# Kernel tuning notes

Hardware: AMD Instinct MI355X
Metric: run time of the kernel (lower is better)

The kernel has to match this reference:

```python
import jax, jax.numpy as jnp
import numpy as np

B, N, C = 16, 1024, 256
NH, DH = 8, 32          # dense attention heads
NHD, P = 8, 4           # deformable heads / sampling points
Hs = Ws = 32            # value spatial grid (N == Hs*Ws)
HID = 1024              # mlp hidden = 4*C


def setup_inputs() -> dict:
    key = jax.random.key(0)
    ks = jax.random.split(key, 16)
    rn = lambda i, shape, s=1.0: jax.random.normal(ks[i], shape, jnp.float32) * s
    return {
        "x": rn(0, (B, N, C)),
        "ref": jax.random.uniform(ks[1], (B, N, 2), jnp.float32),
        "value": rn(2, (B, N, C)),
        "ln1_w": jnp.ones((C,), jnp.float32), "ln1_b": jnp.zeros((C,), jnp.float32),
        "ln2_w": jnp.ones((C,), jnp.float32), "ln2_b": jnp.zeros((C,), jnp.float32),
        "ln3_w": jnp.ones((C,), jnp.float32), "ln3_b": jnp.zeros((C,), jnp.float32),
        "qkv_w": rn(3, (3 * C, C), 0.05),
        "proj_w": rn(4, (C, C), 0.05), "proj_b": jnp.zeros((C,), jnp.float32),
        "off_w": rn(5, (NHD * P * 2, C), 0.01), "off_b": rn(6, (NHD * P * 2,), 0.5),
        "aw_w": rn(7, (NHD * P, C), 0.01), "aw_b": jnp.zeros((NHD * P,), jnp.float32),
        "vproj_w": rn(8, (C, C), 0.05), "vproj_b": jnp.zeros((C,), jnp.float32),
        "oproj_w": rn(9, (C, C), 0.05), "oproj_b": jnp.zeros((C,), jnp.float32),
        "fc1_w": rn(10, (HID, C), 0.05), "fc1_b": jnp.zeros((HID,), jnp.float32),
        "fc2_w": rn(11, (C, HID), 0.05), "fc2_b": jnp.zeros((C,), jnp.float32),
    }


def _ln(x, w, b):
    m = x.mean(-1, keepdims=True)
    v = ((x - m) ** 2).mean(-1, keepdims=True)
    return (x - m) * jax.lax.rsqrt(v + 1e-5) * w + b


def _attn(x, qkv_w, proj_w, proj_b):
    qkv = (x @ qkv_w.T).reshape(B, N, 3, NH, DH)
    q, k, v = qkv[:, :, 0], qkv[:, :, 1], qkv[:, :, 2]
    a = jnp.einsum('bqhd,bkhd->bhqk', q, k) * (DH ** -0.5)
    a = jax.nn.softmax(a, axis=-1)
    o = jnp.einsum('bhqk,bkhd->bqhd', a, v).reshape(B, N, C)
    return o @ proj_w.T + proj_b


def _deform(q, ref, value, off_w, off_b, aw_w, aw_b, vproj_w, vproj_b, oproj_w, oproj_b):
    # single-level MS deformable attention (Deformable-DETR style)
    v = (value @ vproj_w.T + vproj_b).reshape(B, Hs * Ws, NHD, DH)
    off = (q @ off_w.T + off_b).reshape(B, N, NHD, P, 2)
    aw = jax.nn.softmax((q @ aw_w.T + aw_b).reshape(B, N, NHD, P), axis=-1)
    norm = jnp.array([Ws, Hs], jnp.float32)
    loc = ref[:, :, None, None, :] + off / norm  # [B,N,NHD,P,2] normalized coords
    gx = loc[..., 0] * Ws - 0.5
    gy = loc[..., 1] * Hs - 0.5
    x0 = jnp.floor(gx); y0 = jnp.floor(gy)
    lx = gx - x0; ly = gy - y0
    x0i = x0.astype(jnp.int32); y0i = y0.astype(jnp.int32)
    b_idx = jnp.arange(B)[:, None, None, None]
    h_idx = jnp.arange(NHD)[None, None, :, None]

    def gather(xi, yi):
        valid = ((xi >= 0) & (xi < Ws) & (yi >= 0) & (yi < Hs)).astype(jnp.float32)
        idx = jnp.clip(yi, 0, Hs - 1) * Ws + jnp.clip(xi, 0, Ws - 1)
        return v[b_idx, idx, h_idx] * valid[..., None]  # [B,N,NHD,P,DH]

    s = (gather(x0i, y0i) * ((1 - lx) * (1 - ly))[..., None]
         + gather(x0i + 1, y0i) * (lx * (1 - ly))[..., None]
         + gather(x0i, y0i + 1) * ((1 - lx) * ly)[..., None]
         + gather(x0i + 1, y0i + 1) * (lx * ly)[..., None])
    out = (s * aw[..., None]).sum(axis=3).reshape(B, N, C)
    return out @ oproj_w.T + oproj_b


def reference(x, ref, value, ln1_w, ln1_b, ln2_w, ln2_b, ln3_w, ln3_b,
              qkv_w, proj_w, proj_b, off_w, off_b, aw_w, aw_b,
              vproj_w, vproj_b, oproj_w, oproj_b, fc1_w, fc1_b, fc2_w, fc2_b):
    x = x + _attn(_ln(x, ln1_w, ln1_b), qkv_w, proj_w, proj_b)
    x = x + _deform(_ln(x, ln2_w, ln2_b), ref, value,
                    off_w, off_b, aw_w, aw_b, vproj_w, vproj_b, oproj_w, oproj_b)
    h = jax.nn.gelu(_ln(x, ln3_w, ln3_b) @ fc1_w.T + fc1_b, approximate=False) @ fc2_w.T + fc2_b
    return x + h
```

## Files before the change

### kernel.cpp

```cpp
#include <hip/hip_runtime.h>
#include <hip/hip_bf16.h>

#define Bq   16
#define Nq   1024
#define Cq   256
#define NHq  8
#define DHq  32
#define HIDq 1024
#define BNq  (Bq * Nq)

typedef float f32x4 __attribute__((ext_vector_type(4)));
typedef short bf16x8 __attribute__((ext_vector_type(8)));
typedef unsigned short ushort_t;

__device__ __forceinline__ unsigned int f2bf(float f) {
    unsigned int u = __builtin_bit_cast(unsigned int, f);
    u = (u + 0x7fffu + ((u >> 16) & 1u)) >> 16;
    return u & 0xffffu;
}
__device__ __forceinline__ unsigned int packbf2(float a, float b) {
    unsigned int ua = __builtin_bit_cast(unsigned int, a) + 0x8000u;
    unsigned int ub = __builtin_bit_cast(unsigned int, b) + 0x8000u;
    return __builtin_amdgcn_perm(ub, ua, 0x07060302);
}
__device__ __forceinline__ float bflo(unsigned int u) { return __builtin_bit_cast(float, u << 16); }
__device__ __forceinline__ float bfhi(unsigned int u) { return __builtin_bit_cast(float, u & 0xffff0000u); }
__device__ __forceinline__ float gelu_t(float x) {
    float y = x * (0.7978845608028654f + 0.035677408136300125f * x * x);
    float e = __builtin_amdgcn_exp2f(y * 2.8853900817779268f);
    return x - x / (1.f + e);
}

typedef __attribute__((address_space(1))) const unsigned int* gas_u32;
typedef __attribute__((address_space(3))) unsigned int* las_u32;
__device__ __forceinline__ void gload16(const void* g, void* l) {
    __builtin_amdgcn_global_load_lds((gas_u32)g, (las_u32)l, 16, 0, 0);
}

struct CastSeg { const float* src; ushort_t* dst; int nblk; int n; };
struct CastArgs { CastSeg s[9]; };

__global__ __launch_bounds__(256) void castm(CastArgs a) {
    int bid = blockIdx.x;
    int seg = 0, acc = 0;
    for (seg = 0; seg < 9; seg++) {
        if (bid < acc + a.s[seg].nblk) break;
        acc += a.s[seg].nblk;
    }
    const CastSeg sg = a.s[seg];
    int i = (bid - acc) * 1024 + threadIdx.x * 4;
    if (i < sg.n) {
        float4 v = *(const float4*)(sg.src + i);
        uint2 u;
        u.x = packbf2(v.x, v.y);
        u.y = packbf2(v.z, v.w);
        *(uint2*)(sg.dst + i) = u;
    }
}

template <typename TI>
__global__ __launch_bounds__(256) void ln_kernel(const TI* __restrict__ X,
                                                 const float* __restrict__ w,
                                                 const float* __restrict__ b,
                                                 ushort_t* __restrict__ Y) {
    int wave = threadIdx.x >> 6, lane = threadIdx.x & 63;
    int t = blockIdx.x * 4 + wave;
    float4 v;
    if constexpr (sizeof(TI) == 4) {
        v = *(const float4*)((const float*)X + (size_t)t * Cq + lane * 4);
    } else {
        uint2 u = *(const uint2*)((const ushort_t*)X + (size_t)t * Cq + lane * 4);
        v = make_float4(bflo(u.x), bfhi(u.x), bflo(u.y), bfhi(u.y));
    }
    float s = v.x + v.y + v.z + v.w;
#pragma unroll
    for (int d = 1; d < 64; d <<= 1) s += __shfl_xor(s, d);
    float mean = s * (1.f / 256.f);
    float4 dv = {v.x - mean, v.y - mean, v.z - mean, v.w - mean};
    float q = dv.x * dv.x + dv.y * dv.y + dv.z * dv.z + dv.w * dv.w;
#pragma unroll
    for (int d = 1; d < 64; d <<= 1) q += __shfl_xor(q, d);
    float rs = rsqrtf(q * (1.f / 256.f) + 1e-5f);
    float4 wv = *(const float4*)(w + lane * 4);
    float4 bv = *(const float4*)(b + lane * 4);
    uint2 u;
    u.x = packbf2(dv.x * rs * wv.x + bv.x, dv.y * rs * wv.y + bv.y);
    u.y = packbf2(dv.z * rs * wv.z + bv.z, dv.w * rs * wv.w + bv.w);
    *(uint2*)(Y + (size_t)t * Cq + lane * 4) = u;
}

template <int OMODE, bool GELU_, bool RESID, int KT, int NT, typename RT>
__global__ __launch_bounds__(256) void mgemm(const ushort_t* __restrict__ A,
                                             const ushort_t* __restrict__ W,
                                             const float* __restrict__ bias,
                                             const void* __restrict__ R,
                                             void* __restrict__ OutP,
                                             int M, int Nn) {
    constexpr int NJ = NT / 32;
    __shared__ __align__(16) ushort_t Al[8192];
    __shared__ __align__(16) ushort_t Bl[NT * 64];
    int m0 = blockIdx.x * 128, n0 = blockIdx.y * NT;
    int tid = threadIdx.x;
    int w = tid >> 6, lane = tid & 63;
    int l15 = lane & 15, quad = lane >> 4;
    int wrow = w >> 1, wcol = w & 1;

    f32x4 acc[4][NJ];
#pragma unroll
    for (int i = 0; i < 4; i++)
#pragma unroll
        for (int j = 0; j < NJ; j++) acc[i][j] = (f32x4){0.f, 0.f, 0.f, 0.f};

    const ushort_t* gA0 = A + (size_t)(m0 + lane) * KT + w * 8;
    const ushort_t* gA1 = A + (size_t)(m0 + 64 + lane) * KT + w * 8;
    const ushort_t* gB0 = W + (size_t)(n0 + lane) * KT + w * 8;
    const ushort_t* gB1 = (NT == 128) ? W + (size_t)(n0 + 64 + lane) * KT + w * 8 : nullptr;
    ushort_t* lA0  = &Al[(w * 128) * 8];
    ushort_t* lA1  = &Al[(w * 128 + 64) * 8];
    ushort_t* lA0h = &Al[((w + 4) * 128) * 8];
    ushort_t* lA1h = &Al[((w + 4) * 128 + 64) * 8];
    ushort_t* lB0  = &Bl[(w * NT) * 8];
    ushort_t* lB0h = &Bl[((w + 4) * NT) * 8];
    ushort_t* lB1  = (NT == 128) ? &Bl[(w * NT + 64) * 8] : nullptr;
    ushort_t* lB1h = (NT == 128) ? &Bl[((w + 4) * NT + 64) * 8] : nullptr;

#pragma unroll
    for (int k0 = 0; k0 < KT; k0 += 64) {
        gload16(gA0 + k0, lA0);
        gload16(gA1 + k0, lA1);
        gload16(gA0 + k0 + 32, lA0h);
        gload16(gA1 + k0 + 32, lA1h);
        gload16(gB0 + k0, lB0);
        gload16(gB0 + k0 + 32, lB0h);
        if constexpr (NT == 128) {
            gload16(gB1 + k0, lB1);
            gload16(gB1 + k0 + 32, lB1h);
        }
        __syncthreads();

#pragma unroll
        for (int ks = 0; ks < 2; ks++) {
            bf16x8 aF[4], bF[NJ];
#pragma unroll
            for (int i = 0; i < 4; i++)
                aF[i] = *(const bf16x8*)&Al[((ks * 4 + quad) * 128 + wrow * 64 + i * 16 + l15) * 8];
#pragma unroll
            for (int j = 0; j < NJ; j++)
                bF[j] = *(const bf16x8*)&Bl[((ks * 4 + quad) * NT + wcol * (NT / 2) + j * 16 + l15) * 8];
#pragma unroll
            for (int i = 0; i < 4; i++)
#pragma unroll
                for (int j = 0; j < NJ; j++)
                    acc[i][j] = __builtin_amdgcn_mfma_f32_16x16x32_bf16(bF[j], aF[i], acc[i][j], 0, 0, 0);
        }
        __syncthreads();
    }

#pragma unroll
    for (int i = 0; i < 4; i++) {
        int mg = m0 + wrow * 64 + i * 16 + l15;
#pragma unroll
        for (int j = 0; j < NJ; j++) {
            int ng = n0 + wcol * (NT / 2) + j * 16 + quad * 4;
            f32x4 rv = acc[i][j];
            if constexpr (OMODE == 1) {
                int which = ng >> 8;
                int h = (ng >> 5) & 7;
                int d = ng & 31;
                int bb = mg >> 10, nn = mg & 1023;
                ushort_t* qb = (ushort_t*)OutP;
                if (which == 2) {
                    size_t dst = 2 * (size_t)BNq * Cq +
                                 ((size_t)(bb * 8 + h) * 32 + d) * 1024 + nn;
#pragma unroll
                    for (int r = 0; r < 4; r++)
                        qb[dst + (size_t)r * 1024] = (ushort_t)f2bf(rv[r]);
                } else {
                    if (which == 0) {
                        const float sc = 0.17677669529663687f * 1.4426950408889634f;
                        rv[0] *= sc; rv[1] *= sc; rv[2] *= sc; rv[3] *= sc;
                    }
                    size_t dst = (size_t)which * ((size_t)BNq * Cq) +
                                 ((size_t)(bb * 8 + h) * 1024 + nn) * 32 + d;
                    uint2 pk;
                    pk.x = packbf2(rv[0], rv[1]);
                    pk.y = packbf2(rv[2], rv[3]);
                    *(uint2*)(qb + dst) = pk;
                }
            } else if constexpr (OMODE == 3) {
                if (ng >= 96) continue;
                if (ng < 64) {
                    float4 bv = *(const float4*)(bias + ng);
                    rv[0] += bv.x; rv[1] += bv.y; rv[2] += bv.z; rv[3] += bv.w;
                    *(float4*)((float*)OutP + (size_t)mg * 64 + ng) =
                        make_float4(rv[0], rv[1], rv[2], rv[3]);
                } else {
                    float4 bv = *(const float4*)((const float*)R + (ng - 64));
                    rv[0] += bv.x; rv[1] += bv.y; rv[2] += bv.z; rv[3] += bv.w;
                    *(float4*)((float*)OutP + (size_t)BNq * 64 + (size_t)mg * 32 + (ng - 64)) =
                        make_float4(rv[0], rv[1], rv[2], rv[3]);
                }
            } else {
                if (bias) {
                    float4 bv = *(const float4*)(bias + ng);
                    rv[0] += bv.x; rv[1] += bv.y; rv[2] += bv.z; rv[3] += bv.w;
                }
                if (GELU_) {
#pragma unroll
                    for (int r = 0; r < 4; r++) rv[r] = gelu_t(rv[r]);
                }
                if (RESID) {
                    if constexpr (sizeof(RT) == 4) {
                        float4 rr = *(const float4*)((const float*)R + (size_t)mg * Nn + ng);
                        rv[0] += rr.x; rv[1] += rr.y; rv[2] += rr.z; rv[3] += rr.w;
                    } else {
                        uint2 ru = *(const uint2*)((const ushort_t*)R + (size_t)mg * Nn + ng);
                        rv[0] += bflo(ru.x); rv[1] += bfhi(ru.x);
                        rv[2] += bflo(ru.y); rv[3] += bfhi(ru.y);
                    }
                }
                if constexpr (OMODE == 2) {
                    uint2 pk;
                    pk.x = packbf2(rv[0], rv[1]);
                    pk.y = packbf2(rv[2], rv[3]);
                    *(uint2*)((ushort_t*)OutP + (size_t)mg * Nn + ng) = pk;
                } else {
                    *(float4*)((float*)OutP + (size_t)mg * Nn + ng) =
                        make_float4(rv[0], rv[1], rv[2], rv[3]);
                }
            }
        }
    }
}

__global__ __launch_bounds__(256) void attn_mfma(const ushort_t* __restrict__ Qb,
                                                 const ushort_t* __restrict__ Kb,
                                                 const ushort_t* __restrict__ Vtg,
                                                 ushort_t* __restrict__ o) {
    int bh = blockIdx.x;
    int b = bh >> 3, h = bh & 7;
    int q0 = blockIdx.y * 128;
    int tid = threadIdx.x;
    int wave = tid >> 6, lane = tid & 63;
    int l15 = lane & 15, quad = lane >> 4;

    __shared__ __align__(16) ushort_t Ks[64][40];
    __shared__ __align__(16) ushort_t Vs[32][88];
    __shared__ __align__(16) ushort_t Ps[4][32][72];

    const size_t hb = (size_t)bh * 32768;

    bf16x8 qfrag[2];
#pragma unroll
    for (int g = 0; g < 2; g++)
        qfrag[g] = *(const bf16x8*)(Qb + hb + (size_t)(q0 + wave * 32 + g * 16 + l15) * 32 + quad * 8);

    f32x4 oa[2][2];
#pragma unroll
    for (int g = 0; g < 2; g++)
#pragma unroll
        for (int t = 0; t < 2; t++) oa[g][t] = (f32x4){0.f, 0.f, 0.f, 0.f};
    float lsum[2] = {0.f, 0.f};

    int krow = tid >> 2, kch = tid & 3;
    int vrow = tid >> 3, vch = tid & 7;
    const ushort_t* kgp = Kb + hb + (size_t)krow * 32 + kch * 8;
    const ushort_t* vgp = Vtg + hb + (size_t)vrow * 1024 + vch * 8;

    for (int kt = 0; kt < 16; kt++) {
        __syncthreads();
        *(bf16x8*)&Ks[krow][kch * 8] = *(const bf16x8*)(kgp + kt * 64 * 32);
        *(bf16x8*)&Vs[vrow][vch * 8] = *(const bf16x8*)(vgp + kt * 64);
        __syncthreads();

        bf16x8 kf[4];
#pragma unroll
        for (int kg = 0; kg < 4; kg++)
            kf[kg] = *(const bf16x8*)&Ks[kg * 16 + l15][quad * 8];

        const f32x4 z = {0.f, 0.f, 0.f, 0.f};
#pragma unroll
        for (int g = 0; g < 2; g++) {
#pragma unroll
            for (int kg = 0; kg < 4; kg++) {
                f32x4 st = __builtin_amdgcn_mfma_f32_16x16x32_bf16(kf[kg], qfrag[g], z, 0, 0, 0);
                float e0 = __builtin_amdgcn_exp2f(st[0]);
                float e1 = __builtin_amdgcn_exp2f(st[1]);
                float e2 = __builtin_amdgcn_exp2f(st[2]);
                float e3 = __builtin_amdgcn_exp2f(st[3]);
                lsum[g] += (e0 + e1) + (e2 + e3);
                uint2 pk;
                pk.x = packbf2(e0, e1);
                pk.y = packbf2(e2, e3);
                *(uint2*)&Ps[wave][g * 16 + l15][kg * 16 + quad * 4] = pk;
            }
        }
#pragma unroll
        for (int c = 0; c < 2; c++) {
            bf16x8 vb0 = *(const bf16x8*)&Vs[l15][c * 32 + quad * 8];
            bf16x8 vb1 = *(const bf16x8*)&Vs[16 + l15][c * 32 + quad * 8];
#pragma unroll
            for (int g = 0; g < 2; g++) {
                bf16x8 pa = *(const bf16x8*)&Ps[wave][g * 16 + l15][c * 32 + quad * 8];
                oa[g][0] = __builtin_amdgcn_mfma_f32_16x16x32_bf16(pa, vb0, oa[g][0], 0, 0, 0);
                oa[g][1] = __builtin_amdgcn_mfma_f32_16x16x32_bf16(pa, vb1, oa[g][1], 0, 0, 0);
            }
        }
    }

#pragma unroll
    for (int g = 0; g < 2; g++) {
        float rs = lsum[g];
        rs += __shfl_xor(rs, 16);
        rs += __shfl_xor(rs, 32);
        lsum[g] = rs;
    }
#pragma unroll
    for (int g = 0; g < 2; g++) {
#pragma unroll
        for (int r = 0; r < 4; r++) {
            float inv = 1.f / __shfl(lsum[g], quad * 4 + r);
            int q = q0 + wave * 32 + g * 16 + quad * 4 + r;
            ushort_t* orow = o + ((size_t)(b * 1024 + q)) * 256 + h * 32;
            orow[l15] = (ushort_t)f2bf(oa[g][0][r] * inv);
            orow[l15 + 16] = (ushort_t)f2bf(oa[g][1][r] * inv);
        }
    }
}

__global__ __launch_bounds__(256) void deform_kernel(const float* __restrict__ ref,
                                                     const float* __restrict__ off,
                                                     const float* __restrict__ awl,
                                                     const ushort_t* __restrict__ v,
                                                     ushort_t* __restrict__ out) {
    int t = blockIdx.x;
    int b = t >> 10;
    int tid = threadIdx.x;
    int h = tid >> 5, d = tid & 31;

    float rx = ref[(size_t)t * 2 + 0];
    float ry = ref[(size_t)t * 2 + 1];
    const float* offr = off + (size_t)t * 64 + h * 8;
    const float* awr = awl + (size_t)t * 32 + h * 4;

    float L0 = awr[0], L1 = awr[1], L2 = awr[2], L3 = awr[3];
    float mm = fmaxf(fmaxf(L0, L1), fmaxf(L2, L3));
    float e0 = __expf(L0 - mm), e1 = __expf(L1 - mm), e2 = __expf(L2 - mm), e3 = __expf(L3 - mm);
    float inv = 1.f / (e0 + e1 + e2 + e3);
    float aw[4] = {e0 * inv, e1 * inv, e2 * inv, e3 * inv};

    const ushort_t* vb = v + (size_t)b * Nq * Cq + h * 32 + d;

    float s = 0.f;
#pragma unroll
    for (int p = 0; p < 4; p++) {
        float gx = rx * 32.f + offr[p * 2 + 0] - 0.5f;
        float gy = ry * 32.f + offr[p * 2 + 1] - 0.5f;
        float x0f = floorf(gx), y0f = floorf(gy);
        float lx = gx - x0f, ly = gy - y0f;
        int x0 = (int)x0f, y0 = (int)y0f;
        auto g = [&](int xi, int yi) -> float {
            if (xi < 0 || xi > 31 || yi < 0 || yi > 31) return 0.f;
            return bflo((unsigned int)vb[(size_t)(yi * 32 + xi) * Cq]);
        };
        float sp = g(x0, y0) * (1.f - lx) * (1.f - ly)
                 + g(x0 + 1, y0) * lx * (1.f - ly)
                 + g(x0, y0 + 1) * (1.f - lx) * ly
                 + g(x0 + 1, y0 + 1) * lx * ly;
        s += aw[p] * sp;
    }
    out[(size_t)t * Cq + h * 32 + d] = (ushort_t)f2bf(s);
}

extern "C" void kernel_launch(void* const* d_in, const int* in_sizes, int n_in,
                              void* d_out, int out_size, void* d_ws, size_t ws_size,
                              hipStream_t stream) {
    const size_t S = (size_t)BNq * Cq;
    float* ws = (float*)d_ws;
    ushort_t* Xbf = (ushort_t*)ws;
    ushort_t* Ybf = (ushort_t*)(ws + S / 2);
    ushort_t* Wbf = (ushort_t*)(ws + S);

    ushort_t* Wqkv   = Wbf;
    ushort_t* Wproj  = Wbf + 196608;
    ushort_t* Woff   = Wbf + 262144;
    ushort_t* Wvproj = Wbf + 286720;
    ushort_t* Woproj = Wbf + 352256;
    ushort_t* Wfc1   = Wbf + 417792;
    ushort_t* Wfc2   = Wbf + 679936;

    ushort_t* QKVbf = (ushort_t*)(ws + 2 * S);
    ushort_t* O1bf  = (ushort_t*)(ws + 2 * S + 3 * S / 2);
    ushort_t* Vbbf  = (ushort_t*)(ws + 2 * S);
    float* OffB = ws + 2 * S + S / 2;
    float* AwB  = OffB + (size_t)BNq * 64;
    ushort_t* Sbbf = (ushort_t*)(ws + 3 * S);
    ushort_t* Hbbf = (ushort_t*)(ws + 2 * S);
    ushort_t* Valbf = (ushort_t*)(ws + 9 * S / 2);

    auto fp = [&](int i) { return (const float*)d_in[i]; };
    const float* x_in = fp(0);

    CastArgs ca;
    ca.s[0] = {fp(9),  Wqkv,   192, 196608};
    ca.s[1] = {fp(10), Wproj,  64,  65536};
    ca.s[2] = {fp(12), Woff,   16,  16384};
    ca.s[3] = {fp(14), Wbf + 278528, 8, 8192};
    ca.s[4] = {fp(16), Wvproj, 64,  65536};
    ca.s[5] = {fp(18), Woproj, 64,  65536};
    ca.s[6] = {fp(20), Wfc1,   256, 262144};
    ca.s[7] = {fp(22), Wfc2,   256, 262144};
    ca.s[8] = {fp(2),  Valbf,  4096, (int)S};
    castm<<<5016, 256, 0, stream>>>(ca);

    ln_kernel<float><<<BNq / 4, 256, 0, stream>>>(x_in, fp(3), fp(4), Ybf);
    mgemm<1, false, false, 256, 128, float><<<dim3(128, 6), 256, 0, stream>>>(
        Ybf, Wqkv, nullptr, nullptr, QKVbf, BNq, 768);
    attn_mfma<<<dim3(128, 8), 256, 0, stream>>>(
        QKVbf, QKVbf + S, QKVbf + 2 * S, O1bf);
    mgemm<2, false, true, 256, 64, float><<<dim3(128, 4), 256, 0, stream>>>(
        O1bf, Wproj, fp(11), x_in, Xbf, BNq, 256);

    ln_kernel<ushort_t><<<BNq / 4, 256, 0, stream>>>(Xbf, fp(5), fp(6), Ybf);
    mgemm<2, false, false, 256, 64, float><<<dim3(128, 4), 256, 0, stream>>>(
        Valbf, Wvproj, fp(17), nullptr, Vbbf, BNq, 256);
    mgemm<3, false, false, 256, 64, float><<<dim3(128, 2), 256, 0, stream>>>(
        Ybf, Woff, fp(13), fp(15), OffB, BNq, 96);
    deform_kernel<<<BNq, 256, 0, stream>>>(fp(1), OffB, AwB, Vbbf, Sbbf);
    mgemm<2, false, true, 256, 64, ushort_t><<<dim3(128, 4), 256, 0, stream>>>(
        Sbbf, Woproj, fp(19), Xbf, Xbf, BNq, 256);

    ln_kernel<ushort_t><<<BNq / 4, 256, 0, stream>>>(Xbf, fp(7), fp(8), Ybf);
    mgemm<2, true, false, 256, 128, float><<<dim3(128, 8), 256, 0, stream>>>(
        Ybf, Wfc1, fp(21), nullptr, Hbbf, BNq, 1024);
    mgemm<0, false, true, 1024, 64, ushort_t><<<dim3(128, 4), 256, 0, stream>>>(
        Hbbf, Wfc2, fp(23), Xbf, d_out, BNq, 256);
}
```

Baseline: 357.6 us.

## Double-buffer GEMM LDS stages and prefetch K/V tiles in attention

The GEMM kernel now keeps two LDS buffers and issues the global-to-LDS loads for the next K slice before computing the current one, with one barrier per iteration instead of two. The tile width is fixed at 64 columns, so the QKV and FC1 GEMMs launch twice as many blocks. The attention kernel loads the next K/V tile into registers while the current tile is being consumed. The aim is to hide global memory latency behind MFMA work, at the cost of more LDS per block and more redundant A-tile loads for the wide GEMMs.

After: 368.2 us. +3.0%, slower.

```diff
diff --git a/kernel.cpp b/kernel.cpp
--- a/kernel.cpp
+++ b/kernel.cpp
@@ -89,79 +89,70 @@
     *(uint2*)(Y + (size_t)t * Cq + lane * 4) = u;
 }
 
-template <int OMODE, bool GELU_, bool RESID, int KT, int NT, typename RT>
+template <int OMODE, bool GELU_, bool RESID, int KT, typename RT>
 __global__ __launch_bounds__(256) void mgemm(const ushort_t* __restrict__ A,
                                              const ushort_t* __restrict__ W,
                                              const float* __restrict__ bias,
                                              const void* __restrict__ R,
                                              void* __restrict__ OutP,
                                              int M, int Nn) {
-    constexpr int NJ = NT / 32;
-    __shared__ __align__(16) ushort_t Al[8192];
-    __shared__ __align__(16) ushort_t Bl[NT * 64];
-    int m0 = blockIdx.x * 128, n0 = blockIdx.y * NT;
+    __shared__ __align__(16) ushort_t Al[2][8192];
+    __shared__ __align__(16) ushort_t Bl[2][4096];
+    int m0 = blockIdx.x * 128, n0 = blockIdx.y * 64;
     int tid = threadIdx.x;
     int w = tid >> 6, lane = tid & 63;
     int l15 = lane & 15, quad = lane >> 4;
     int wrow = w >> 1, wcol = w & 1;
 
-    f32x4 acc[4][NJ];
+    f32x4 acc[4][2];
 #pragma unroll
     for (int i = 0; i < 4; i++)
 #pragma unroll
-        for (int j = 0; j < NJ; j++) acc[i][j] = (f32x4){0.f, 0.f, 0.f, 0.f};
+        for (int j = 0; j < 2; j++) acc[i][j] = (f32x4){0.f, 0.f, 0.f, 0.f};
 
     const ushort_t* gA0 = A + (size_t)(m0 + lane) * KT + w * 8;
     const ushort_t* gA1 = A + (size_t)(m0 + 64 + lane) * KT + w * 8;
     const ushort_t* gB0 = W + (size_t)(n0 + lane) * KT + w * 8;
-    const ushort_t* gB1 = (NT == 128) ? W + (size_t)(n0 + 64 + lane) * KT + w * 8 : nullptr;
-    ushort_t* lA0  = &Al[(w * 128) * 8];
-    ushort_t* lA1  = &Al[(w * 128 + 64) * 8];
-    ushort_t* lA0h = &Al[((w + 4) * 128) * 8];
-    ushort_t* lA1h = &Al[((w + 4) * 128 + 64) * 8];
-    ushort_t* lB0  = &Bl[(w * NT) * 8];
-    ushort_t* lB0h = &Bl[((w + 4) * NT) * 8];
-    ushort_t* lB1  = (NT == 128) ? &Bl[(w * NT + 64) * 8] : nullptr;
-    ushort_t* lB1h = (NT == 128) ? &Bl[((w + 4) * NT + 64) * 8] : nullptr;
-
-#pragma unroll
-    for (int k0 = 0; k0 < KT; k0 += 64) {
-        gload16(gA0 + k0, lA0);
-        gload16(gA1 + k0, lA1);
-        gload16(gA0 + k0 + 32, lA0h);
-        gload16(gA1 + k0 + 32, lA1h);
-        gload16(gB0 + k0, lB0);
-        gload16(gB0 + k0 + 32, lB0h);
-        if constexpr (NT == 128) {
-            gload16(gB1 + k0, lB1);
-            gload16(gB1 + k0 + 32, lB1h);
-        }
+
+    auto stage = [&](int k0, int buf) {
+        gload16(gA0 + k0,      &Al[buf][(w * 128) * 8]);
+        gload16(gA1 + k0,      &Al[buf][(w * 128 + 64) * 8]);
+        gload16(gA0 + k0 + 32, &Al[buf][((w + 4) * 128) * 8]);
+        gload16(gA1 + k0 + 32, &Al[buf][((w + 4) * 128 + 64) * 8]);
+        gload16(gB0 + k0,      &Bl[buf][(w * 64) * 8]);
+        gload16(gB0 + k0 + 32, &Bl[buf][((w + 4) * 64) * 8]);
+    };
+
+    stage(0, 0);
+    constexpr int NIT = KT / 64;
+#pragma unroll
+    for (int it = 0; it < NIT; it++) {
         __syncthreads();
-
+        if (it + 1 < NIT) stage((it + 1) * 64, (it + 1) & 1);
+        const int buf = it & 1;
 #pragma unroll
         for (int ks = 0; ks < 2; ks++) {
-            bf16x8 aF[4], bF[NJ];
+            bf16x8 aF[4], bF[2];
 #pragma unroll
             for (int i = 0; i < 4; i++)
-                aF[i] = *(const bf16x8*)&Al[((ks * 4 + quad) * 128 + wrow * 64 + i * 16 + l15) * 8];
-#pragma unroll
-            for (int j = 0; j < NJ; j++)
-                bF[j] = *(const bf16x8*)&Bl[((ks * 4 + quad) * NT + wcol * (NT / 2) + j * 16 + l15) * 8];
+                aF[i] = *(const bf16x8*)&Al[buf][((ks * 4 + quad) * 128 + wrow * 64 + i * 16 + l15) * 8];
+#pragma unroll
+            for (int j = 0; j < 2; j++)
+                bF[j] = *(const bf16x8*)&Bl[buf][((ks * 4 + quad) * 64 + wcol * 32 + j * 16 + l15) * 8];
 #pragma unroll
             for (int i = 0; i < 4; i++)
 #pragma unroll
-                for (int j = 0; j < NJ; j++)
+                for (int j = 0; j < 2; j++)
                     acc[i][j] = __builtin_amdgcn_mfma_f32_16x16x32_bf16(bF[j], aF[i], acc[i][j], 0, 0, 0);
         }
-        __syncthreads();
     }
 
 #pragma unroll
     for (int i = 0; i < 4; i++) {
         int mg = m0 + wrow * 64 + i * 16 + l15;
 #pragma unroll
-        for (int j = 0; j < NJ; j++) {
-            int ng = n0 + wcol * (NT / 2) + j * 16 + quad * 4;
+        for (int j = 0; j < 2; j++) {
+            int ng = n0 + wcol * 32 + j * 16 + quad * 4;
             f32x4 rv = acc[i][j];
             if constexpr (OMODE == 1) {
                 int which = ng >> 8;
@@ -267,11 +258,18 @@
     const ushort_t* kgp = Kb + hb + (size_t)krow * 32 + kch * 8;
     const ushort_t* vgp = Vtg + hb + (size_t)vrow * 1024 + vch * 8;
 
+    bf16x8 kreg = *(const bf16x8*)(kgp);
+    bf16x8 vreg = *(const bf16x8*)(vgp);
+
     for (int kt = 0; kt < 16; kt++) {
         __syncthreads();
-        *(bf16x8*)&Ks[krow][kch * 8] = *(const bf16x8*)(kgp + kt * 64 * 32);
-        *(bf16x8*)&Vs[vrow][vch * 8] = *(const bf16x8*)(vgp + kt * 64);
+        *(bf16x8*)&Ks[krow][kch * 8] = kreg;
+        *(bf16x8*)&Vs[vrow][vch * 8] = vreg;
         __syncthreads();
+        if (kt < 15) {
+            kreg = *(const bf16x8*)(kgp + (size_t)(kt + 1) * 2048);
+            vreg = *(const bf16x8*)(vgp + (kt + 1) * 64);
+        }
 
         bf16x8 kf[4];
 #pragma unroll
@@ -414,25 +412,25 @@
     castm<<<5016, 256, 0, stream>>>(ca);
 
     ln_kernel<float><<<BNq / 4, 256, 0, stream>>>(x_in, fp(3), fp(4), Ybf);
-    mgemm<1, false, false, 256, 128, float><<<dim3(128, 6), 256, 0, stream>>>(
+    mgemm<1, false, false, 256, float><<<dim3(128, 12), 256, 0, stream>>>(
         Ybf, Wqkv, nullptr, nullptr, QKVbf, BNq, 768);
     attn_mfma<<<dim3(128, 8), 256, 0, stream>>>(
         QKVbf, QKVbf + S, QKVbf + 2 * S, O1bf);
-    mgemm<2, false, true, 256, 64, float><<<dim3(128, 4), 256, 0, stream>>>(
+    mgemm<2, false, true, 256, float><<<dim3(128, 4), 256, 0, stream>>>(
         O1bf, Wproj, fp(11), x_in, Xbf, BNq, 256);
 
     ln_kernel<ushort_t><<<BNq / 4, 256, 0, stream>>>(Xbf, fp(5), fp(6), Ybf);
-    mgemm<2, false, false, 256, 64, float><<<dim3(128, 4), 256, 0, stream>>>(
+    mgemm<2, false, false, 256, float><<<dim3(128, 4), 256, 0, stream>>>(
         Valbf, Wvproj, fp(17), nullptr, Vbbf, BNq, 256);
-    mgemm<3, false, false, 256, 64, float><<<dim3(128, 2), 256, 0, stream>>>(
+    mgemm<3, false, false, 256, float><<<dim3(128, 2), 256, 0, stream>>>(
         Ybf, Woff, fp(13), fp(15), OffB, BNq, 96);
     deform_kernel<<<BNq, 256, 0, stream>>>(fp(1), OffB, AwB, Vbbf, Sbbf);
-    mgemm<2, false, true, 256, 64, ushort_t><<<dim3(128, 4), 256, 0, stream>>>(
+    mgemm<2, false, true, 256, ushort_t><<<dim3(128, 4), 256, 0, stream>>>(
         Sbbf, Woproj, fp(19), Xbf, Xbf, BNq, 256);
 
     ln_kernel<ushort_t><<<BNq / 4, 256, 0, stream>>>(Xbf, fp(7), fp(8), Ybf);
-    mgemm<2, true, false, 256, 128, float><<<dim3(128, 8), 256, 0, stream>>>(
+    mgemm<2, true, false, 256, float><<<dim3(128, 16), 256, 0, stream>>>(
         Ybf, Wfc1, fp(21), nullptr, Hbbf, BNq, 1024);
-    mgemm<0, false, true, 1024, 64, ushort_t><<<dim3(128, 4), 256, 0, stream>>>(
+    mgemm<0, false, true, 1024, ushort_t><<<dim3(128, 4), 256, 0, stream>>>(
         Hbbf, Wfc2, fp(23), Xbf, d_out, BNq, 256);
 }
```
